# Kernel optimization log

Measured on AMD Instinct MI355X. Metric: run time of the kernel, lower is better.

## Reference

```python
import jax, jax.numpy as jnp
import numpy as np

B, S, D, F_, E, K = 64, 8, 2048, 4096, 8, 2


def setup_inputs() -> dict:
    key = jax.random.key(0)
    ks = jax.random.split(key, 5)
    scale_in = 1.0 / np.sqrt(D)
    scale_ff = 1.0 / np.sqrt(F_)
    return {
        "x": jax.random.normal(ks[0], (B, S, D), dtype=jnp.float32),
        "gate_w": jax.random.normal(ks[1], (D, E), dtype=jnp.float32) * scale_in,
        "w1": jax.random.normal(ks[2], (E, D, F_), dtype=jnp.float32) * scale_in,
        "w3": jax.random.normal(ks[3], (E, D, F_), dtype=jnp.float32) * scale_in,
        "w2": jax.random.normal(ks[4], (E, F_, D), dtype=jnp.float32) * scale_ff,
        "top_k": K,
    }


def reference(x, gate_w, w1, w3, w2, top_k):
    # x: [B,S,D]; gate_w: [D,E]; w1,w3: [E,D,F]; w2: [E,F,D]
    n_experts = gate_w.shape[-1]
    gate_logits = jnp.einsum("bsd,de->bse", x, gate_w)          # [B,S,E]
    weights, selected = jax.lax.top_k(gate_logits, top_k)        # [B,S,K]
    weights = jax.nn.softmax(weights, axis=-1)                   # softmax over k (dim=2)
    # per-token combine weight for every expert: [B,S,E]
    combine = jnp.einsum(
        "bsk,bske->bse", weights, jax.nn.one_hot(selected, n_experts, dtype=x.dtype)
    )
    # SwiGLU expert FFN, batched over the (small, fixed) expert axis
    h = jax.nn.silu(jnp.einsum("bsd,edf->ebsf", x, w1)) * jnp.einsum(
        "bsd,edf->ebsf", x, w3
    )                                                            # [E,B,S,F]
    expert_out = jnp.einsum("ebsf,efd->ebsd", h, w2)             # [E,B,S,D]
    return jnp.einsum("bse,ebsd->bsd", combine, expert_out)      # [B,S,D]
```

## Files before the change

### kernel.cpp

```cpp
#include <hip/hip_runtime.h>
#include <hip/hip_bf16.h>
#include <cstdint>
#include <cstddef>

#define NB   64
#define NS   8
#define DIM  2048
#define FF   4096
#define NE   8
#define TOK  512
#define NPAIR 1024

#define BM   192
#define BN   64
#define BK   32

typedef __attribute__((ext_vector_type(4))) float f32x4;
typedef __attribute__((ext_vector_type(8))) short bf16x8;
typedef __attribute__((ext_vector_type(4))) short bf16x4;

#define MFMA16(a, b, c) __builtin_amdgcn_mfma_f32_16x16x32_bf16((a), (b), (c), 0, 0, 0)

#define VMCNT8  asm volatile("s_waitcnt vmcnt(8)" ::: "memory")
#define VMCNT4  asm volatile("s_waitcnt vmcnt(4)" ::: "memory")
#define VMCNT0  asm volatile("s_waitcnt vmcnt(0)" ::: "memory")
#define LGKMBAR do { asm volatile("s_waitcnt lgkmcnt(0)" ::: "memory"); \
                     asm volatile("s_barrier" ::: "memory");            \
                     __builtin_amdgcn_sched_barrier(0); } while (0)
#define SCHEDBAR __builtin_amdgcn_sched_barrier(0)

static __device__ __forceinline__ short f2bf(float f) {
    unsigned u = __builtin_bit_cast(unsigned, f);
    return (short)((u + 0x8000u) >> 16);
}

static __device__ __forceinline__ void async16(void* l, const void* g) {
    __builtin_amdgcn_global_load_lds(
        (const __attribute__((address_space(1))) void*)g,
        (__attribute__((address_space(3))) void*)l, 16, 0, 0);
}

__global__ void gate_topk(const float* __restrict__ x, const float* __restrict__ gw,
                          unsigned short* __restrict__ xbf,
                          int* __restrict__ tok_expert, float* __restrict__ tok_gatew) {
    int token = blockIdx.x;
    int lane  = threadIdx.x;
    const float* xr = x + (size_t)token * DIM;

    float acc[NE];
#pragma unroll
    for (int e = 0; e < NE; ++e) acc[e] = 0.f;

    for (int d0 = lane * 8; d0 < DIM; d0 += 64 * 8) {
        float4 xa = *(const float4*)(xr + d0);
        float4 xb = *(const float4*)(xr + d0 + 4);
        bf16x8 v;
        v[0] = f2bf(xa.x); v[1] = f2bf(xa.y); v[2] = f2bf(xa.z); v[3] = f2bf(xa.w);
        v[4] = f2bf(xb.x); v[5] = f2bf(xb.y); v[6] = f2bf(xb.z); v[7] = f2bf(xb.w);
        *(bf16x8*)(xbf + (size_t)token * DIM + d0) = v;
#pragma unroll
        for (int j = 0; j < 8; ++j) {
            float xv = (j < 4) ? ((const float*)&xa)[j] : ((const float*)&xb)[j - 4];
            const float4* g = (const float4*)(gw + (size_t)(d0 + j) * NE);
            float4 g0 = g[0], g1 = g[1];
            acc[0] += xv * g0.x; acc[1] += xv * g0.y;
            acc[2] += xv * g0.z; acc[3] += xv * g0.w;
            acc[4] += xv * g1.x; acc[5] += xv * g1.y;
            acc[6] += xv * g1.z; acc[7] += xv * g1.w;
        }
    }
#pragma unroll
    for (int off = 32; off >= 1; off >>= 1) {
#pragma unroll
        for (int e = 0; e < NE; ++e) acc[e] += __shfl_down(acc[e], off);
    }
    if (lane == 0) {
        float b1 = -1e30f, b2 = -1e30f; int i1 = 0, i2 = 0;
#pragma unroll
        for (int e = 0; e < NE; ++e) {
            float v = acc[e];
            if (v > b1) { b2 = b1; i2 = i1; b1 = v; i1 = e; }
            else if (v > b2) { b2 = v; i2 = e; }
        }
        float t = __expf(b2 - b1);
        tok_expert[token * 2 + 0] = i1;
        tok_expert[token * 2 + 1] = i2;
        tok_gatew[token * 2 + 0] = 1.f / (1.f + t);
        tok_gatew[token * 2 + 1] = t / (1.f + t);
    }
}

__global__ void build_lists(const int* __restrict__ tok_expert,
                            const float* __restrict__ tok_gatew,
                            int* __restrict__ counts, int* __restrict__ offsets,
                            int* __restrict__ row_token, float* __restrict__ row_gatew,
                            int* __restrict__ pair_row) {
    __shared__ int s_off[NE];
    __shared__ int s_cnt[NE];
    int e    = threadIdx.x >> 6;
    int lane = threadIdx.x & 63;
    unsigned long long lt = (1ull << lane) - 1ull;

    int cnt = 0;
    for (int base = 0; base < NPAIR; base += 64) {
        int id = tok_expert[base + lane];
        unsigned long long m = __ballot(id == e);
        cnt += __popcll(m);
    }
    if (lane == 0) s_cnt[e] = cnt;
    __syncthreads();
    if (threadIdx.x == 0) {
        int o = 0;
        for (int i = 0; i < NE; ++i) {
            int c = s_cnt[i];
            counts[i] = c; offsets[i] = o; s_off[i] = o; o += c;
        }
    }
    __syncthreads();

    int rbase = s_off[e];
    for (int base = 0; base < NPAIR; base += 64) {
        int entry = base + lane;
        int id = tok_expert[entry];
        bool match = (id == e);
        unsigned long long m = __ballot(match);
        int pre = __popcll(m & lt);
        if (match) {
            int row = rbase + pre;
            row_token[row] = entry >> 1;
            row_gatew[row] = tok_gatew[entry];
            pair_row[entry] = row;
        }
        rbase += __popcll(m);
    }
}

#define EPOCH1(P, W, L, S, IA, IB) do {                                       \
    if (IA) stageA((P) ^ 1, ((S) + 1) * BK);                                  \
    SCHEDBAR;                                                                 \
    if (IB) {                                                                 \
        _Pragma("unroll")                                                     \
        for (int j = 0; j < 8; ++j)                                           \
            L[j] = bbase[((size_t)((S) + 2) * BK + j) * FF];                  \
    }                                                                         \
    bf16x8 a_[3];                                                             \
    _Pragma("unroll")                                                         \
    for (int f = 0; f < 3; ++f) {                                             \
        int m_ = wm * 48 + f * 16 + l15;                                      \
        a_[f] = *(const bf16x8*)&As[P][(size_t)m_ * BK + ((lg ^ (m_ & 3)) << 3)]; \
    }                                                                         \
    _Pragma("unroll")                                                         \
    for (int nf = 0; nf < 2; ++nf) {                                          \
        int ch_ = (wn * 32 + nf * 16 + l15) + (lg << 6);                      \
        bf16x8 b1_ = *(const bf16x8*)&Bs[P][0][ch_ * 8];                      \
        bf16x8 b3_ = *(const bf16x8*)&Bs[P][1][ch_ * 8];                      \
        _Pragma("unroll")                                                     \
        for (int f = 0; f < 3; ++f) {                                         \
            acc1[f][nf] = MFMA16(a_[f], b1_, acc1[f][nf]);                    \
            acc3[f][nf] = MFMA16(a_[f], b3_, acc3[f][nf]);                    \
        }                                                                     \
    }                                                                         \
    if (IA) {                                                                 \
        bf16x8 wv_;                                                           \
        _Pragma("unroll")                                                     \
        for (int j = 0; j < 8; ++j) wv_[j] = f2bf(W[j]);                      \
        *(bf16x8*)&Bs[(P) ^ 1][bmat][bchunk * 8] = wv_;                       \
    }                                                                         \
    if (IB) { VMCNT8; } else if (IA) { VMCNT0; }                              \
    LGKMBAR;                                                                  \
} while (0)

__global__ __launch_bounds__(512, 4) void ffn1(
    const unsigned short* __restrict__ xbf, const float* __restrict__ w1,
    const float* __restrict__ w3,
    const int* __restrict__ counts, const int* __restrict__ offsets,
    const int* __restrict__ row_token, unsigned short* __restrict__ Hbuf) {
    __shared__ __align__(16) unsigned short As[2][BM * BK];
    __shared__ __align__(16) unsigned short Bs[2][2][2048];

    int bid = blockIdx.x;
    int e  = bid >> 6;
    int f0 = (bid & 63) * BN;

    int Me = counts[e];
    if (Me == 0) return;
    int off = offsets[e];

    int t = threadIdx.x;
    int lane = t & 63;
    int w = t >> 6;
    int wm = w >> 1, wn = w & 1;
    int l15 = lane & 15, lg = lane >> 4;

    const float* w1e = w1 + (size_t)e * DIM * FF + f0;
    const float* w3e = w3 + (size_t)e * DIM * FF + f0;

    int bmat = t >> 8;
    int bchunk = t & 255;
    int bcol = bchunk & 63, blg = bchunk >> 6;
    const float* bbase = (bmat ? w3e : w1e) + (size_t)(blg * 8) * FF + bcol;

    const int NSTG = DIM / BK;

    for (int mb = 0; mb < Me; mb += BM) {
        const unsigned short* asrc0;
        const unsigned short* asrc1;
        {
            int m0 = t >> 2, c0 = t & 3;
            int rl0 = mb + m0;
            int tok0 = row_token[off + ((rl0 < Me) ? rl0 : (Me - 1))];
            asrc0 = xbf + (size_t)tok0 * DIM + ((c0 ^ (m0 & 3)) << 3);
            int i1 = 512 + t;
            int m1 = i1 >> 2, c1 = i1 & 3;
            int rl1 = mb + m1;
            int tok1 = row_token[off + ((rl1 < Me) ? rl1 : (Me - 1))];
            asrc1 = xbf + (size_t)tok1 * DIM + ((c1 ^ (m1 & 3)) << 3);
        }

        f32x4 acc1[3][2], acc3[3][2];
#pragma unroll
        for (int f = 0; f < 3; ++f)
#pragma unroll
            for (int nf = 0; nf < 2; ++nf) {
                acc1[f][nf] = (f32x4){0.f, 0.f, 0.f, 0.f};
                acc3[f][nf] = (f32x4){0.f, 0.f, 0.f, 0.f};
            }

        auto stageA = [&](int buf, int k0) {
            async16(&As[buf][(size_t)t * 8], asrc0 + k0);
            if (t < 256) async16(&As[buf][(size_t)(512 + t) * 8], asrc1 + k0);
        };

        float bX[8], bY[8];
        stageA(0, 0);
        SCHEDBAR;
#pragma unroll
        for (int j = 0; j < 8; ++j) bX[j] = bbase[(size_t)j * FF];
#pragma unroll
        for (int j = 0; j < 8; ++j) bY[j] = bbase[((size_t)BK + j) * FF];
        {
            bf16x8 wv;
#pragma unroll
            for (int j = 0; j < 8; ++j) wv[j] = f2bf(bX[j]);
            *(bf16x8*)&Bs[0][bmat][bchunk * 8] = wv;
        }
        VMCNT8;
        LGKMBAR;

        for (int s = 0; s < NSTG - 2; s += 2) {
            EPOCH1(0, bY, bX, s, 1, 1);
            EPOCH1(1, bX, bY, s + 1, 1, 1);
        }
        EPOCH1(0, bY, bX, NSTG - 2, 1, 0);
        EPOCH1(1, bX, bY, NSTG - 1, 0, 0);

#pragma unroll
        for (int f = 0; f < 3; ++f)
#pragma unroll
            for (int nf = 0; nf < 2; ++nf)
#pragma unroll
                for (int r = 0; r < 4; ++r) {
                    int rl = mb + wm * 48 + f * 16 + lg * 4 + r;
                    if (rl < Me) {
                        float a1 = acc1[f][nf][r], a3 = acc3[f][nf][r];
                        float h = (a1 / (1.f + __expf(-a1))) * a3;
                        Hbuf[(size_t)(off + rl) * FF + f0 + wn * 32 + nf * 16 + l15] =
                            (unsigned short)f2bf(h);
                    }
                }
    }
}

#define EPOCH2(P, W, L, S, IA, IB) do {                                       \
    if (IA) stageA((P) ^ 1, ((S) + 1) * BK);                                  \
    SCHEDBAR;                                                                 \
    if (IB) {                                                                 \
        _Pragma("unroll")                                                     \
        for (int j = 0; j < 4; ++j)                                           \
            L[j] = bbase[((size_t)((S) + 2) * BK + j) * DIM];                 \
    }                                                                         \
    bf16x8 a_[3];                                                             \
    _Pragma("unroll")                                                         \
    for (int f = 0; f < 3; ++f) {                                             \
        int m_ = wm * 48 + f * 16 + l15;                                      \
        a_[f] = *(const bf16x8*)&As[P][(size_t)m_ * BK + ((lg ^ (m_ & 3)) << 3)]; \
    }                                                                         \
    _Pragma("unroll")                                                         \
    for (int nf = 0; nf < 2; ++nf) {                                          \
        int ch_ = (wn * 32 + nf * 16 + l15) + (lg << 6);                      \
        bf16x8 bw_ = *(const bf16x8*)&Bs[P][ch_ * 8];                         \
        _Pragma("unroll")                                                     \
        for (int f = 0; f < 3; ++f)                                           \
            acc[f][nf] = MFMA16(a_[f], bw_, acc[f][nf]);                      \
    }                                                                         \
    if (IA) {                                                                 \
        bf16x4 wv_;                                                           \
        _Pragma("unroll")                                                     \
        for (int j = 0; j < 4; ++j) wv_[j] = f2bf(W[j]);                      \
        *(bf16x4*)&Bs[(P) ^ 1][bchunk * 8 + bhalf * 4] = wv_;                 \
    }                                                                         \
    if (IB) { VMCNT4; } else if (IA) { VMCNT0; }                              \
    LGKMBAR;                                                                  \
} while (0)

__global__ __launch_bounds__(512, 4) void ffn2(
    const unsigned short* __restrict__ Hbuf, const float* __restrict__ w2,
    const int* __restrict__ counts, const int* __restrict__ offsets,
    const float* __restrict__ row_gatew, float* __restrict__ OP) {
    __shared__ __align__(16) unsigned short As[2][BM * BK];
    __shared__ __align__(16) unsigned short Bs[2][2048];

    int bid = blockIdx.x;
    int e  = bid >> 5;
    int d0 = (bid & 31) * BN;

    int Me = counts[e];
    if (Me == 0) return;
    int off = offsets[e];

    int t = threadIdx.x;
    int lane = t & 63;
    int w = t >> 6;
    int wm = w >> 1, wn = w & 1;
    int l15 = lane & 15, lg = lane >> 4;

    const float* w2e = w2 + (size_t)e * FF * DIM + d0;

    int bchunk = t & 255;
    int bhalf  = t >> 8;
    int bcol = bchunk & 63, blg = bchunk >> 6;
    const float* bbase = w2e + (size_t)(blg * 8 + bhalf * 4) * DIM + bcol;

    const int NSTG = FF / BK;

    for (int mb = 0; mb < Me; mb += BM) {
        const unsigned short* asrc0;
        const unsigned short* asrc1;
        {
            int m0 = t >> 2, c0 = t & 3;
            int rl0 = mb + m0;
            asrc0 = Hbuf + (size_t)(off + ((rl0 < Me) ? rl0 : (Me - 1))) * FF
                         + ((c0 ^ (m0 & 3)) << 3);
            int i1 = 512 + t;
            int m1 = i1 >> 2, c1 = i1 & 3;
            int rl1 = mb + m1;
            asrc1 = Hbuf + (size_t)(off + ((rl1 < Me) ? rl1 : (Me - 1))) * FF
                         + ((c1 ^ (m1 & 3)) << 3);
        }

        f32x4 acc[3][2];
#pragma unroll
        for (int f = 0; f < 3; ++f)
#pragma unroll
            for (int nf = 0; nf < 2; ++nf) acc[f][nf] = (f32x4){0.f, 0.f, 0.f, 0.f};

        auto stageA = [&](int buf, int k0) {
            async16(&As[buf][(size_t)t * 8], asrc0 + k0);
            if (t < 256) async16(&As[buf][(size_t)(512 + t) * 8], asrc1 + k0);
        };

        float bX[4], bY[4];
        stageA(0, 0);
        SCHEDBAR;
#pragma unroll
        for (int j = 0; j < 4; ++j) bX[j] = bbase[(size_t)j * DIM];
#pragma unroll
        for (int j = 0; j < 4; ++j) bY[j] = bbase[((size_t)BK + j) * DIM];
        {
            bf16x4 wv;
#pragma unroll
            for (int j = 0; j < 4; ++j) wv[j] = f2bf(bX[j]);
            *(bf16x4*)&Bs[0][bchunk * 8 + bhalf * 4] = wv;
        }
        VMCNT4;
        LGKMBAR;

        for (int s = 0; s < NSTG - 2; s += 2) {
            EPOCH2(0, bY, bX, s, 1, 1);
            EPOCH2(1, bX, bY, s + 1, 1, 1);
        }
        EPOCH2(0, bY, bX, NSTG - 2, 1, 0);
        EPOCH2(1, bX, bY, NSTG - 1, 0, 0);

#pragma unroll
        for (int f = 0; f < 3; ++f)
#pragma unroll
            for (int nf = 0; nf < 2; ++nf)
#pragma unroll
                for (int r = 0; r < 4; ++r) {
                    int rl = mb + wm * 48 + f * 16 + lg * 4 + r;
                    if (rl < Me) {
                        int grow = off + rl;
                        float g = row_gatew[grow];
                        OP[(size_t)grow * DIM + d0 + wn * 32 + nf * 16 + l15] =
                            acc[f][nf][r] * g;
                    }
                }
    }
}

__global__ void combine(const float* __restrict__ OP, const int* __restrict__ pair_row,
                        float* __restrict__ out) {
    int idx = blockIdx.x * blockDim.x + threadIdx.x;
    int token = idx >> 9;
    int q = idx & 511;
    int r0 = pair_row[token * 2 + 0];
    int r1 = pair_row[token * 2 + 1];
    float4 a = *(const float4*)(OP + (size_t)r0 * DIM + q * 4);
    float4 b = *(const float4*)(OP + (size_t)r1 * DIM + q * 4);
    float4 o;
    o.x = a.x + b.x; o.y = a.y + b.y; o.z = a.z + b.z; o.w = a.w + b.w;
    *(float4*)(out + (size_t)token * DIM + q * 4) = o;
}

extern "C" void kernel_launch(void* const* d_in, const int* in_sizes, int n_in,
                              void* d_out, int out_size, void* d_ws, size_t ws_size,
                              hipStream_t stream) {
    const float* x  = (const float*)d_in[0];
    const float* gw = (const float*)d_in[1];
    const float* w1 = (const float*)d_in[2];
    const float* w3 = (const float*)d_in[3];
    const float* w2 = (const float*)d_in[4];
    float* out = (float*)d_out;

    char* ws = (char*)d_ws;
    unsigned short* Hbuf = (unsigned short*)ws;
    float* OP            = (float*)(ws + 8388608);
    unsigned short* xbf  = (unsigned short*)(ws + 16777216);
    char* meta           = ws + 18874368;
    int*   tok_expert = (int*)(meta);
    float* tok_gatew  = (float*)(meta + 4096);
    int*   counts     = (int*)(meta + 8192);
    int*   offsets    = (int*)(meta + 8224);
    int*   row_token  = (int*)(meta + 8256);
    float* row_gatew  = (float*)(meta + 12352);
    int*   pair_row   = (int*)(meta + 16448);

    gate_topk<<<TOK, 64, 0, stream>>>(x, gw, xbf, tok_expert, tok_gatew);
    build_lists<<<1, 512, 0, stream>>>(tok_expert, tok_gatew, counts, offsets,
                                       row_token, row_gatew, pair_row);
    ffn1<<<NE * 64, 512, 0, stream>>>(xbf, w1, w3, counts, offsets, row_token, Hbuf);
    ffn2<<<NE * 32, 512, 0, stream>>>(Hbuf, w2, counts, offsets, row_gatew, OP);
    combine<<<1024, 256, 0, stream>>>(OP, pair_row, out);
}
```

Measured before the change: 236.6 us.

## Load A operands directly to registers, narrow N tile, double grid for expert GEMMs

Both expert GEMM kernels stop staging the activation tile through LDS with async global-to-LDS loads. Each wave now loads its A fragments straight from global memory into registers, double-buffered across k-steps. The tiles become BM=256 with one wave per 32 rows, BN=32 and BK=64, and the grids double so more blocks stream the fp32 weights in parallel. The aim is to spread the weight-bandwidth-bound work over more CUs and drop the LDS traffic for A. The cost is redundant A loads from global or cache across blocks, and the explicit vmcnt waits are removed in favour of compiler-inserted ones.

New measurement: 276.9 us. 1.17x slower.

```diff
diff --git a/kernel.cpp b/kernel.cpp
--- a/kernel.cpp
+++ b/kernel.cpp
@@ -11,33 +11,23 @@
 #define TOK  512
 #define NPAIR 1024
 
-#define BM   192
-#define BN   64
-#define BK   32
+#define BM   256
+#define BN   32
+#define BKE  64
 
 typedef __attribute__((ext_vector_type(4))) float f32x4;
 typedef __attribute__((ext_vector_type(8))) short bf16x8;
 typedef __attribute__((ext_vector_type(4))) short bf16x4;
 
 #define MFMA16(a, b, c) __builtin_amdgcn_mfma_f32_16x16x32_bf16((a), (b), (c), 0, 0, 0)
-
-#define VMCNT8  asm volatile("s_waitcnt vmcnt(8)" ::: "memory")
-#define VMCNT4  asm volatile("s_waitcnt vmcnt(4)" ::: "memory")
-#define VMCNT0  asm volatile("s_waitcnt vmcnt(0)" ::: "memory")
+#define SCHEDBAR __builtin_amdgcn_sched_barrier(0)
 #define LGKMBAR do { asm volatile("s_waitcnt lgkmcnt(0)" ::: "memory"); \
                      asm volatile("s_barrier" ::: "memory");            \
                      __builtin_amdgcn_sched_barrier(0); } while (0)
-#define SCHEDBAR __builtin_amdgcn_sched_barrier(0)
 
 static __device__ __forceinline__ short f2bf(float f) {
     unsigned u = __builtin_bit_cast(unsigned, f);
     return (short)((u + 0x8000u) >> 16);
-}
-
-static __device__ __forceinline__ void async16(void* l, const void* g) {
-    __builtin_amdgcn_global_load_lds(
-        (const __attribute__((address_space(1))) void*)g,
-        (__attribute__((address_space(3))) void*)l, 16, 0, 0);
 }
 
 __global__ void gate_topk(const float* __restrict__ x, const float* __restrict__ gw,
@@ -135,38 +125,49 @@
     }
 }
 
-#define EPOCH1(P, W, L, S, IA, IB) do {                                       \
-    if (IA) stageA((P) ^ 1, ((S) + 1) * BK);                                  \
+#define EPOCH1(CUR, AC, AN, WS, LS, S, DO_AN, DO_L, DO_W) do {                \
+    if (DO_AN) {                                                              \
+        _Pragma("unroll")                                                     \
+        for (int f = 0; f < 2; ++f) {                                         \
+            AN[f]     = *(const bf16x8*)(arow[f] + ((S) + 1) * BKE);          \
+            AN[2 + f] = *(const bf16x8*)(arow[f] + ((S) + 1) * BKE + 32);     \
+        }                                                                     \
+    }                                                                         \
     SCHEDBAR;                                                                 \
-    if (IB) {                                                                 \
+    if (DO_L) {                                                               \
         _Pragma("unroll")                                                     \
         for (int j = 0; j < 8; ++j)                                           \
-            L[j] = bbase[((size_t)((S) + 2) * BK + j) * FF];                  \
-    }                                                                         \
-    bf16x8 a_[3];                                                             \
-    _Pragma("unroll")                                                         \
-    for (int f = 0; f < 3; ++f) {                                             \
-        int m_ = wm * 48 + f * 16 + l15;                                      \
-        a_[f] = *(const bf16x8*)&As[P][(size_t)m_ * BK + ((lg ^ (m_ & 3)) << 3)]; \
-    }                                                                         \
+            LS[j] = bsrc[(size_t)(((S) + 2) * BKE + j) * FF];                 \
+    }                                                                         \
+    SCHEDBAR;                                                                 \
     _Pragma("unroll")                                                         \
     for (int nf = 0; nf < 2; ++nf) {                                          \
-        int ch_ = (wn * 32 + nf * 16 + l15) + (lg << 6);                      \
-        bf16x8 b1_ = *(const bf16x8*)&Bs[P][0][ch_ * 8];                      \
-        bf16x8 b3_ = *(const bf16x8*)&Bs[P][1][ch_ * 8];                      \
-        _Pragma("unroll")                                                     \
-        for (int f = 0; f < 3; ++f) {                                         \
-            acc1[f][nf] = MFMA16(a_[f], b1_, acc1[f][nf]);                    \
-            acc3[f][nf] = MFMA16(a_[f], b3_, acc3[f][nf]);                    \
+        int ch = nf * 16 + l15 + lg * 32;                                     \
+        bf16x8 b1f = *(const bf16x8*)&Bs[CUR][0][0][ch][0];                   \
+        bf16x8 b3f = *(const bf16x8*)&Bs[CUR][1][0][ch][0];                   \
+        _Pragma("unroll")                                                     \
+        for (int f = 0; f < 2; ++f) {                                         \
+            acc1[f][nf] = MFMA16(AC[f], b1f, acc1[f][nf]);                    \
+            acc3[f][nf] = MFMA16(AC[f], b3f, acc3[f][nf]);                    \
         }                                                                     \
     }                                                                         \
-    if (IA) {                                                                 \
-        bf16x8 wv_;                                                           \
-        _Pragma("unroll")                                                     \
-        for (int j = 0; j < 8; ++j) wv_[j] = f2bf(W[j]);                      \
-        *(bf16x8*)&Bs[(P) ^ 1][bmat][bchunk * 8] = wv_;                       \
-    }                                                                         \
-    if (IB) { VMCNT8; } else if (IA) { VMCNT0; }                              \
+    _Pragma("unroll")                                                         \
+    for (int nf = 0; nf < 2; ++nf) {                                          \
+        int ch = nf * 16 + l15 + lg * 32;                                     \
+        bf16x8 b1f = *(const bf16x8*)&Bs[CUR][0][1][ch][0];                   \
+        bf16x8 b3f = *(const bf16x8*)&Bs[CUR][1][1][ch][0];                   \
+        _Pragma("unroll")                                                     \
+        for (int f = 0; f < 2; ++f) {                                         \
+            acc1[f][nf] = MFMA16(AC[2 + f], b1f, acc1[f][nf]);                \
+            acc3[f][nf] = MFMA16(AC[2 + f], b3f, acc3[f][nf]);                \
+        }                                                                     \
+    }                                                                         \
+    if (DO_W) {                                                               \
+        bf16x8 wv;                                                            \
+        _Pragma("unroll")                                                     \
+        for (int j = 0; j < 8; ++j) wv[j] = f2bf(WS[j]);                      \
+        *(bf16x8*)&Bs[(CUR) ^ 1][bmat][bsl][bch][0] = wv;                     \
+    }                                                                         \
     LGKMBAR;                                                                  \
 } while (0)
 
@@ -175,12 +176,11 @@
     const float* __restrict__ w3,
     const int* __restrict__ counts, const int* __restrict__ offsets,
     const int* __restrict__ row_token, unsigned short* __restrict__ Hbuf) {
-    __shared__ __align__(16) unsigned short As[2][BM * BK];
-    __shared__ __align__(16) unsigned short Bs[2][2][2048];
+    __shared__ __align__(16) unsigned short Bs[2][2][2][128][8];
 
     int bid = blockIdx.x;
-    int e  = bid >> 6;
-    int f0 = (bid & 63) * BN;
+    int e  = bid >> 7;
+    int f0 = (bid & 127) * BN;
 
     int Me = counts[e];
     if (Me == 0) return;
@@ -188,118 +188,117 @@
 
     int t = threadIdx.x;
     int lane = t & 63;
-    int w = t >> 6;
-    int wm = w >> 1, wn = w & 1;
+    int wm = t >> 6;
     int l15 = lane & 15, lg = lane >> 4;
 
     const float* w1e = w1 + (size_t)e * DIM * FF + f0;
     const float* w3e = w3 + (size_t)e * DIM * FF + f0;
 
     int bmat = t >> 8;
-    int bchunk = t & 255;
-    int bcol = bchunk & 63, blg = bchunk >> 6;
-    const float* bbase = (bmat ? w3e : w1e) + (size_t)(blg * 8) * FF + bcol;
-
-    const int NSTG = DIM / BK;
+    int bc   = t & 255;
+    int bsl  = bc >> 7;
+    int blgw = (bc >> 5) & 3;
+    int bcol = bc & 31;
+    const float* bsrc = (bmat ? w3e : w1e) + (size_t)(bsl * 32 + blgw * 8) * FF + bcol;
+    int bch = bcol + blgw * 32;
+
+    const int NST = DIM / BKE;
 
     for (int mb = 0; mb < Me; mb += BM) {
-        const unsigned short* asrc0;
-        const unsigned short* asrc1;
-        {
-            int m0 = t >> 2, c0 = t & 3;
-            int rl0 = mb + m0;
-            int tok0 = row_token[off + ((rl0 < Me) ? rl0 : (Me - 1))];
-            asrc0 = xbf + (size_t)tok0 * DIM + ((c0 ^ (m0 & 3)) << 3);
-            int i1 = 512 + t;
-            int m1 = i1 >> 2, c1 = i1 & 3;
-            int rl1 = mb + m1;
-            int tok1 = row_token[off + ((rl1 < Me) ? rl1 : (Me - 1))];
-            asrc1 = xbf + (size_t)tok1 * DIM + ((c1 ^ (m1 & 3)) << 3);
-        }
-
-        f32x4 acc1[3][2], acc3[3][2];
-#pragma unroll
-        for (int f = 0; f < 3; ++f)
+        const unsigned short* arow[2];
+#pragma unroll
+        for (int f = 0; f < 2; ++f) {
+            int rl = mb + wm * 32 + f * 16 + l15;
+            int rr = (rl < Me) ? rl : (Me - 1);
+            arow[f] = xbf + (size_t)row_token[off + rr] * DIM + lg * 8;
+        }
+
+        f32x4 acc1[2][2], acc3[2][2];
+#pragma unroll
+        for (int f = 0; f < 2; ++f)
 #pragma unroll
             for (int nf = 0; nf < 2; ++nf) {
                 acc1[f][nf] = (f32x4){0.f, 0.f, 0.f, 0.f};
                 acc3[f][nf] = (f32x4){0.f, 0.f, 0.f, 0.f};
             }
 
-        auto stageA = [&](int buf, int k0) {
-            async16(&As[buf][(size_t)t * 8], asrc0 + k0);
-            if (t < 256) async16(&As[buf][(size_t)(512 + t) * 8], asrc1 + k0);
-        };
-
         float bX[8], bY[8];
-        stageA(0, 0);
-        SCHEDBAR;
-#pragma unroll
-        for (int j = 0; j < 8; ++j) bX[j] = bbase[(size_t)j * FF];
-#pragma unroll
-        for (int j = 0; j < 8; ++j) bY[j] = bbase[((size_t)BK + j) * FF];
+        bf16x8 aC[4], aN[4];
+
+#pragma unroll
+        for (int j = 0; j < 8; ++j) bX[j] = bsrc[(size_t)j * FF];
         {
             bf16x8 wv;
 #pragma unroll
             for (int j = 0; j < 8; ++j) wv[j] = f2bf(bX[j]);
-            *(bf16x8*)&Bs[0][bmat][bchunk * 8] = wv;
-        }
-        VMCNT8;
+            *(bf16x8*)&Bs[0][bmat][bsl][bch][0] = wv;
+        }
+#pragma unroll
+        for (int f = 0; f < 2; ++f) {
+            aC[f]     = *(const bf16x8*)(arow[f]);
+            aC[2 + f] = *(const bf16x8*)(arow[f] + 32);
+        }
+        SCHEDBAR;
+#pragma unroll
+        for (int j = 0; j < 8; ++j) bX[j] = bsrc[(size_t)(BKE + j) * FF];
         LGKMBAR;
 
-        for (int s = 0; s < NSTG - 2; s += 2) {
-            EPOCH1(0, bY, bX, s, 1, 1);
-            EPOCH1(1, bX, bY, s + 1, 1, 1);
-        }
-        EPOCH1(0, bY, bX, NSTG - 2, 1, 0);
-        EPOCH1(1, bX, bY, NSTG - 1, 0, 0);
-
-#pragma unroll
-        for (int f = 0; f < 3; ++f)
+        for (int s = 0; s < NST - 2; s += 2) {
+            EPOCH1(0, aC, aN, bX, bY, s, 1, 1, 1);
+            EPOCH1(1, aN, aC, bY, bX, s + 1, 1, 1, 1);
+        }
+        EPOCH1(0, aC, aN, bX, bY, NST - 2, 1, 0, 1);
+        EPOCH1(1, aN, aC, bY, bX, NST - 1, 0, 0, 0);
+
+#pragma unroll
+        for (int f = 0; f < 2; ++f)
 #pragma unroll
             for (int nf = 0; nf < 2; ++nf)
 #pragma unroll
                 for (int r = 0; r < 4; ++r) {
-                    int rl = mb + wm * 48 + f * 16 + lg * 4 + r;
+                    int rl = mb + wm * 32 + f * 16 + lg * 4 + r;
                     if (rl < Me) {
                         float a1 = acc1[f][nf][r], a3 = acc3[f][nf][r];
                         float h = (a1 / (1.f + __expf(-a1))) * a3;
-                        Hbuf[(size_t)(off + rl) * FF + f0 + wn * 32 + nf * 16 + l15] =
+                        Hbuf[(size_t)(off + rl) * FF + f0 + nf * 16 + l15] =
                             (unsigned short)f2bf(h);
                     }
                 }
     }
 }
 
-#define EPOCH2(P, W, L, S, IA, IB) do {                                       \
-    if (IA) stageA((P) ^ 1, ((S) + 1) * BK);                                  \
+#define EPOCH2(CUR, AC, AN, WS, LS, S, DO_AN, DO_L, DO_W) do {                \
+    if (DO_AN) {                                                              \
+        _Pragma("unroll")                                                     \
+        for (int f = 0; f < 2; ++f) {                                         \
+            AN[f]     = *(const bf16x8*)(arow[f] + ((S) + 1) * BKE);          \
+            AN[2 + f] = *(const bf16x8*)(arow[f] + ((S) + 1) * BKE + 32);     \
+        }                                                                     \
+    }                                                                         \
     SCHEDBAR;                                                                 \
-    if (IB) {                                                                 \
+    if (DO_L) {                                                               \
         _Pragma("unroll")                                                     \
         for (int j = 0; j < 4; ++j)                                           \
-            L[j] = bbase[((size_t)((S) + 2) * BK + j) * DIM];                 \
-    }                                                                         \
-    bf16x8 a_[3];                                                             \
-    _Pragma("unroll")                                                         \
-    for (int f = 0; f < 3; ++f) {                                             \
-        int m_ = wm * 48 + f * 16 + l15;                                      \
-        a_[f] = *(const bf16x8*)&As[P][(size_t)m_ * BK + ((lg ^ (m_ & 3)) << 3)]; \
-    }                                                                         \
+            LS[j] = bsrc[(size_t)(((S) + 2) * BKE + j) * DIM];                \
+    }                                                                         \
+    SCHEDBAR;                                                                 \
     _Pragma("unroll")                                                         \
     for (int nf = 0; nf < 2; ++nf) {                                          \
-        int ch_ = (wn * 32 + nf * 16 + l15) + (lg << 6);                      \
-        bf16x8 bw_ = *(const bf16x8*)&Bs[P][ch_ * 8];                         \
-        _Pragma("unroll")                                                     \
-        for (int f = 0; f < 3; ++f)                                           \
-            acc[f][nf] = MFMA16(a_[f], bw_, acc[f][nf]);                      \
-    }                                                                         \
-    if (IA) {                                                                 \
-        bf16x4 wv_;                                                           \
-        _Pragma("unroll")                                                     \
-        for (int j = 0; j < 4; ++j) wv_[j] = f2bf(W[j]);                      \
-        *(bf16x4*)&Bs[(P) ^ 1][bchunk * 8 + bhalf * 4] = wv_;                 \
-    }                                                                         \
-    if (IB) { VMCNT4; } else if (IA) { VMCNT0; }                              \
+        int ch = nf * 16 + l15 + lg * 32;                                     \
+        bf16x8 b0 = *(const bf16x8*)&Bs[CUR][0][ch][0];                       \
+        bf16x8 b1s = *(const bf16x8*)&Bs[CUR][1][ch][0];                      \
+        _Pragma("unroll")                                                     \
+        for (int f = 0; f < 2; ++f) {                                         \
+            acc[f][nf] = MFMA16(AC[f], b0, acc[f][nf]);                       \
+            acc[f][nf] = MFMA16(AC[2 + f], b1s, acc[f][nf]);                  \
+        }                                                                     \
+    }                                                                         \
+    if (DO_W) {                                                               \
+        bf16x4 wv;                                                            \
+        _Pragma("unroll")                                                     \
+        for (int j = 0; j < 4; ++j) wv[j] = f2bf(WS[j]);                      \
+        *(bf16x4*)&Bs[(CUR) ^ 1][bsl][bch][bh * 4] = wv;                      \
+    }                                                                         \
     LGKMBAR;                                                                  \
 } while (0)
 
@@ -307,12 +306,11 @@
     const unsigned short* __restrict__ Hbuf, const float* __restrict__ w2,
     const int* __restrict__ counts, const int* __restrict__ offsets,
     const float* __restrict__ row_gatew, float* __restrict__ OP) {
-    __shared__ __align__(16) unsigned short As[2][BM * BK];
-    __shared__ __align__(16) unsigned short Bs[2][2048];
+    __shared__ __align__(16) unsigned short Bs[2][2][128][8];
 
     int bid = blockIdx.x;
-    int e  = bid >> 5;
-    int d0 = (bid & 31) * BN;
+    int e  = bid >> 6;
+    int d0 = (bid & 63) * BN;
 
     int Me = counts[e];
     if (Me == 0) return;
@@ -320,80 +318,74 @@
 
     int t = threadIdx.x;
     int lane = t & 63;
-    int w = t >> 6;
-    int wm = w >> 1, wn = w & 1;
+    int wm = t >> 6;
     int l15 = lane & 15, lg = lane >> 4;
 
     const float* w2e = w2 + (size_t)e * FF * DIM + d0;
 
-    int bchunk = t & 255;
-    int bhalf  = t >> 8;
-    int bcol = bchunk & 63, blg = bchunk >> 6;
-    const float* bbase = w2e + (size_t)(blg * 8 + bhalf * 4) * DIM + bcol;
-
-    const int NSTG = FF / BK;
+    int bc  = t >> 1, bh = t & 1;
+    int bsl = bc >> 7;
+    int blgw = (bc >> 5) & 3;
+    int bcol = bc & 31;
+    const float* bsrc = w2e + (size_t)(bsl * 32 + blgw * 8 + bh * 4) * DIM + bcol;
+    int bch = bcol + blgw * 32;
+
+    const int NST = FF / BKE;
 
     for (int mb = 0; mb < Me; mb += BM) {
-        const unsigned short* asrc0;
-        const unsigned short* asrc1;
-        {
-            int m0 = t >> 2, c0 = t & 3;
-            int rl0 = mb + m0;
-            asrc0 = Hbuf + (size_t)(off + ((rl0 < Me) ? rl0 : (Me - 1))) * FF
-                         + ((c0 ^ (m0 & 3)) << 3);
-            int i1 = 512 + t;
-            int m1 = i1 >> 2, c1 = i1 & 3;
-            int rl1 = mb + m1;
-            asrc1 = Hbuf + (size_t)(off + ((rl1 < Me) ? rl1 : (Me - 1))) * FF
-                         + ((c1 ^ (m1 & 3)) << 3);
-        }
-
-        f32x4 acc[3][2];
-#pragma unroll
-        for (int f = 0; f < 3; ++f)
+        const unsigned short* arow[2];
+#pragma unroll
+        for (int f = 0; f < 2; ++f) {
+            int rl = mb + wm * 32 + f * 16 + l15;
+            int rr = (rl < Me) ? rl : (Me - 1);
+            arow[f] = Hbuf + (size_t)(off + rr) * FF + lg * 8;
+        }
+
+        f32x4 acc[2][2];
+#pragma unroll
+        for (int f = 0; f < 2; ++f)
 #pragma unroll
             for (int nf = 0; nf < 2; ++nf) acc[f][nf] = (f32x4){0.f, 0.f, 0.f, 0.f};
 
-        auto stageA = [&](int buf, int k0) {
-            async16(&As[buf][(size_t)t * 8], asrc0 + k0);
-            if (t < 256) async16(&As[buf][(size_t)(512 + t) * 8], asrc1 + k0);
-        };
-
         float bX[4], bY[4];
-        stageA(0, 0);
-        SCHEDBAR;
-#pragma unroll
-        for (int j = 0; j < 4; ++j) bX[j] = bbase[(size_t)j * DIM];
-#pragma unroll
-        for (int j = 0; j < 4; ++j) bY[j] = bbase[((size_t)BK + j) * DIM];
+        bf16x8 aC[4], aN[4];
+
+#pragma unroll
+        for (int j = 0; j < 4; ++j) bX[j] = bsrc[(size_t)j * DIM];
         {
             bf16x4 wv;
 #pragma unroll
             for (int j = 0; j < 4; ++j) wv[j] = f2bf(bX[j]);
-            *(bf16x4*)&Bs[0][bchunk * 8 + bhalf * 4] = wv;
-        }
-        VMCNT4;
+            *(bf16x4*)&Bs[0][bsl][bch][bh * 4] = wv;
+        }
+#pragma unroll
+        for (int f = 0; f < 2; ++f) {
+            aC[f]     = *(const bf16x8*)(arow[f]);
+            aC[2 + f] = *(const bf16x8*)(arow[f] + 32);
+        }
+        SCHEDBAR;
+#pragma unroll
+        for (int j = 0; j < 4; ++j) bX[j] = bsrc[(size_t)(BKE + j) * DIM];
         LGKMBAR;
 
-        for (int s = 0; s < NSTG - 2; s += 2) {
-            EPOCH2(0, bY, bX, s, 1, 1);
-            EPOCH2(1, bX, bY, s + 1, 1, 1);
-        }
-        EPOCH2(0, bY, bX, NSTG - 2, 1, 0);
-        EPOCH2(1, bX, bY, NSTG - 1, 0, 0);
-
-#pragma unroll
-        for (int f = 0; f < 3; ++f)
+        for (int s = 0; s < NST - 2; s += 2) {
+            EPOCH2(0, aC, aN, bX, bY, s, 1, 1, 1);
+            EPOCH2(1, aN, aC, bY, bX, s + 1, 1, 1, 1);
+        }
+        EPOCH2(0, aC, aN, bX, bY, NST - 2, 1, 0, 1);
+        EPOCH2(1, aN, aC, bY, bX, NST - 1, 0, 0, 0);
+
+#pragma unroll
+        for (int f = 0; f < 2; ++f)
 #pragma unroll
             for (int nf = 0; nf < 2; ++nf)
 #pragma unroll
                 for (int r = 0; r < 4; ++r) {
-                    int rl = mb + wm * 48 + f * 16 + lg * 4 + r;
+                    int rl = mb + wm * 32 + f * 16 + lg * 4 + r;
                     if (rl < Me) {
                         int grow = off + rl;
                         float g = row_gatew[grow];
-                        OP[(size_t)grow * DIM + d0 + wn * 32 + nf * 16 + l15] =
-                            acc[f][nf][r] * g;
+                        OP[(size_t)grow * DIM + d0 + nf * 16 + l15] = acc[f][nf][r] * g;
                     }
                 }
     }
@@ -439,7 +431,7 @@
     gate_topk<<<TOK, 64, 0, stream>>>(x, gw, xbf, tok_expert, tok_gatew);
     build_lists<<<1, 512, 0, stream>>>(tok_expert, tok_gatew, counts, offsets,
                                        row_token, row_gatew, pair_row);
-    ffn1<<<NE * 64, 512, 0, stream>>>(xbf, w1, w3, counts, offsets, row_token, Hbuf);
-    ffn2<<<NE * 32, 512, 0, stream>>>(Hbuf, w2, counts, offsets, row_gatew, OP);
+    ffn1<<<NE * 128, 512, 0, stream>>>(xbf, w1, w3, counts, offsets, row_token, Hbuf);
+    ffn2<<<NE * 64, 512, 0, stream>>>(Hbuf, w2, counts, offsets, row_gatew, OP);
     combine<<<1024, 256, 0, stream>>>(OP, pair_row, out);
 }
```
